# Kernel tuning notes

Hardware: AMD Instinct MI355X
Metric: run time of the kernel (lower is better)

Reference implementation:

```python
import jax, jax.numpy as jnp
import numpy as np

N_GRIDS = 64
N_FEATURES = 2
GRID_SHAPE = (64, 64, 64)  # (D, H, W)
N_DIMS = 3
N_POINTS = 262144


def setup_inputs() -> dict:
    key = jax.random.key(0)
    k1, k2, k3 = jax.random.split(key, 3)
    # Global query coordinates in [-1, 1]^3
    x = jax.random.uniform(k1, (N_POINTS, N_DIMS), dtype=jnp.float32, minval=-1.0, maxval=1.0)
    # Emulate randomize_grids(): M = (I + 0.1*U on top n_dims rows); M = M @ M^T; zero bottom-left row
    eye = jnp.eye(N_DIMS + 1, dtype=jnp.float32)[None].repeat(N_GRIDS, axis=0)
    noise = jax.random.uniform(k2, (N_GRIDS, N_DIMS, N_DIMS + 1), dtype=jnp.float32) * 0.1
    M = eye.at[:, :N_DIMS, :].add(noise)
    M = jnp.einsum('gij,gkj->gik', M, M)
    M = M.at[:, N_DIMS, :N_DIMS].set(0.0)
    # Feature grids uniform in [-1e-4, 1e-4]
    feature_grids = jax.random.uniform(
        k3, (N_GRIDS, N_FEATURES) + GRID_SHAPE, dtype=jnp.float32,
        minval=-1e-4, maxval=1e-4)
    return {"x": x, "transformation_matrices": M, "feature_grids": feature_grids}


def _trilinear_sample_one_grid(grid, coords):
    """PyTorch-style 3D grid_sample, bilinear, align_corners=True, padding_mode='zeros'.
    grid:   [F, D, H, W]
    coords: [N, 3] with last dim ordered (x, y, z) -> (W, H, D)
    returns [F, N]
    """
    F_, D, H, W = grid.shape
    # align_corners=True: map [-1,1] -> [0, size-1]
    px = (coords[:, 0] + 1.0) * 0.5 * (W - 1)
    py = (coords[:, 1] + 1.0) * 0.5 * (H - 1)
    pz = (coords[:, 2] + 1.0) * 0.5 * (D - 1)
    x0 = jnp.floor(px); y0 = jnp.floor(py); z0 = jnp.floor(pz)
    fx = px - x0; fy = py - y0; fz = pz - z0
    x0 = x0.astype(jnp.int32); y0 = y0.astype(jnp.int32); z0 = z0.astype(jnp.int32)
    out = jnp.zeros((F_, coords.shape[0]), dtype=grid.dtype)
    for dz in (0, 1):
        wz = jnp.where(dz == 1, fz, 1.0 - fz)
        iz = z0 + dz
        vz = (iz >= 0) & (iz < D)
        izc = jnp.clip(iz, 0, D - 1)
        for dy in (0, 1):
            wy = jnp.where(dy == 1, fy, 1.0 - fy)
            iy = y0 + dy
            vy = (iy >= 0) & (iy < H)
            iyc = jnp.clip(iy, 0, H - 1)
            for dx in (0, 1):
                wx = jnp.where(dx == 1, fx, 1.0 - fx)
                ix = x0 + dx
                valid = vz & vy & (ix >= 0) & (ix < W)
                ixc = jnp.clip(ix, 0, W - 1)
                vals = grid[:, izc, iyc, ixc]  # [F, N] gather
                w = (wx * wy * wz) * valid.astype(grid.dtype)
                out = out + vals * w[None, :]
    return out


def reference(x, transformation_matrices, feature_grids):
    N = x.shape[0]
    G, F_ = feature_grids.shape[0], feature_grids.shape[1]
    # transform(): homogeneous coords, batched matmul, drop homogeneous coord
    homog = jnp.concatenate([x, jnp.ones((N, 1), dtype=x.dtype)], axis=1)  # [N, 4]
    pts = jnp.einsum('gij,nj->gni', transformation_matrices, homog)[..., :N_DIMS]  # [G, N, 3]
    pts = jax.lax.stop_gradient(pts)  # forward() detaches the sampling grid
    feats = jax.vmap(_trilinear_sample_one_grid)(feature_grids, pts)  # [G, F, N]
    # flatten(0,-2).permute(1,0) -> [N, G*F]
    return feats.reshape(G * F_, N).T
```

## Files before the change

### kernel.cpp

```cpp
#include <hip/hip_runtime.h>


constexpr int NPTS  = 262144;
constexpr int GVOX  = 64 * 64 * 64;
constexpr int NCELL = 4096;

__global__ __launch_bounds__(256) void repack_kernel(
    const float* __restrict__ src, float4* __restrict__ dst)
{
    int tid = blockIdx.x * 256 + threadIdx.x;
    int g = tid >> 16;
    int q = tid & 65535;
    const float* p0 = src + (size_t)g * (2 * GVOX) + q * 4;
    float4 a = *reinterpret_cast<const float4*>(p0);
    float4 b = *reinterpret_cast<const float4*>(p0 + GVOX);
    float4* o = dst + (((size_t)g * GVOX) >> 1) + (size_t)q * 2;
    o[0] = make_float4(a.x, b.x, a.y, b.y);
    o[1] = make_float4(a.z, b.z, a.w, b.w);
}

__device__ __forceinline__ int cell_id(float x, float y, float z)
{
    int cx = min(max((int)((x + 1.0f) * 8.0f), 0), 15);
    int cy = min(max((int)((y + 1.0f) * 8.0f), 0), 15);
    int cz = min(max((int)((z + 1.0f) * 8.0f), 0), 15);
    int c = 0;
    #pragma unroll
    for (int b = 0; b < 4; ++b)
        c |= (((cx >> b) & 1) << (3 * b))
           | (((cy >> b) & 1) << (3 * b + 1))
           | (((cz >> b) & 1) << (3 * b + 2));
    return c;
}

__global__ __launch_bounds__(256) void zero_hist(int* __restrict__ hist)
{
    hist[blockIdx.x * 256 + threadIdx.x] = 0;
}

__global__ __launch_bounds__(256) void hist_kernel(
    const float* __restrict__ xs, int* __restrict__ hist)
{
    int n = blockIdx.x * 256 + threadIdx.x;
    float x = xs[n * 3 + 0], y = xs[n * 3 + 1], z = xs[n * 3 + 2];
    atomicAdd(&hist[cell_id(x, y, z)], 1);
}

__global__ __launch_bounds__(1024) void scan_kernel(
    const int* __restrict__ hist, int* __restrict__ off)
{
    __shared__ int part[1024];
    int t = threadIdx.x;
    int4 h = reinterpret_cast<const int4*>(hist)[t];
    int s = h.x + h.y + h.z + h.w;
    part[t] = s;
    __syncthreads();
    for (int d = 1; d < 1024; d <<= 1) {
        int v = (t >= d) ? part[t - d] : 0;
        __syncthreads();
        part[t] += v;
        __syncthreads();
    }
    int excl = part[t] - s;
    int4 o;
    o.x = excl;
    o.y = o.x + h.x;
    o.z = o.y + h.y;
    o.w = o.z + h.z;
    reinterpret_cast<int4*>(off)[t] = o;
}

__global__ __launch_bounds__(256) void scatter_kernel(
    const float* __restrict__ xs, int* __restrict__ off,
    float4* __restrict__ sorted)
{
    int n = blockIdx.x * 256 + threadIdx.x;
    float x = xs[n * 3 + 0], y = xs[n * 3 + 1], z = xs[n * 3 + 2];
    int c = cell_id(x, y, z);
    int pos = atomicAdd(&off[c], 1);
    sorted[pos] = make_float4(x, y, z, __int_as_float(n));
}

template <bool PACKED>
__global__ __launch_bounds__(256) void sample_sorted(
    const float4* __restrict__ sorted, const float* __restrict__ Ms,
    const float* __restrict__ grids, float* __restrict__ out)
{
    int blk = blockIdx.x;
    int chunk = ((blk & 7) << 7) + (blk >> 3);

    float4 sp = sorted[chunk * 256 + threadIdx.x];
    const float cx = sp.x, cy = sp.y, cz = sp.z;
    const int n = __float_as_int(sp.w);
    float4* outr = reinterpret_cast<float4*>(out + (size_t)n * 128);

    for (int p = 0; p < 8; ++p) {
        float2 acc[8];
        #pragma unroll
        for (int gg = 0; gg < 8; ++gg) {
            const int g = p * 8 + gg;
            const float* Mg = Ms + g * 16;
            const float px = (fmaf(Mg[0], cx, fmaf(Mg[1], cy, fmaf(Mg[2],  cz, Mg[3])))  + 1.0f) * 31.5f;
            const float py = (fmaf(Mg[4], cx, fmaf(Mg[5], cy, fmaf(Mg[6],  cz, Mg[7])))  + 1.0f) * 31.5f;
            const float pz = (fmaf(Mg[8], cx, fmaf(Mg[9], cy, fmaf(Mg[10], cz, Mg[11]))) + 1.0f) * 31.5f;

            const float flx = floorf(px), fly = floorf(py), flz = floorf(pz);
            const float fx = px - flx, fy = py - fly, fz = pz - flz;
            const int x0 = (int)flx, y0 = (int)fly, z0 = (int)flz;

            const float wx0 = (x0 >= 0  && x0 < 64) ? (1.0f - fx) : 0.0f;
            const float wx1 = (x0 >= -1 && x0 < 63) ? fx          : 0.0f;
            const float wy0 = (y0 >= 0  && y0 < 64) ? (1.0f - fy) : 0.0f;
            const float wy1 = (y0 >= -1 && y0 < 63) ? fy          : 0.0f;
            const float wz0 = (z0 >= 0  && z0 < 64) ? (1.0f - fz) : 0.0f;
            const float wz1 = (z0 >= -1 && z0 < 63) ? fz          : 0.0f;

            const int xc0 = min(max(x0, 0), 63), xc1 = min(max(x0 + 1, 0), 63);
            const int yc0 = min(max(y0, 0), 63), yc1 = min(max(y0 + 1, 0), 63);
            const int zc0 = min(max(z0, 0), 63), zc1 = min(max(z0 + 1, 0), 63);

            const int r00 = (zc0 * 64 + yc0) * 64, r01 = (zc0 * 64 + yc1) * 64;
            const int r10 = (zc1 * 64 + yc0) * 64, r11 = (zc1 * 64 + yc1) * 64;

            const float waa = wz0 * wy0, wab = wz0 * wy1;
            const float wba = wz1 * wy0, wbb = wz1 * wy1;
            const float pA0 = waa * wx0, pA1 = waa * wx1;
            const float pB0 = wab * wx0, pB1 = wab * wx1;
            const float pC0 = wba * wx0, pC1 = wba * wx1;
            const float pD0 = wbb * wx0, pD1 = wbb * wx1;

            float a0, a1;
            if constexpr (PACKED) {
                const float2* gp = reinterpret_cast<const float2*>(grids) + (size_t)g * GVOX;
                const float2 vA0 = gp[r00 + xc0], vA1 = gp[r00 + xc1];
                const float2 vB0 = gp[r01 + xc0], vB1 = gp[r01 + xc1];
                const float2 vC0 = gp[r10 + xc0], vC1 = gp[r10 + xc1];
                const float2 vD0 = gp[r11 + xc0], vD1 = gp[r11 + xc1];
                a0 = vA0.x * pA0 + vA1.x * pA1 + vB0.x * pB0 + vB1.x * pB1
                   + vC0.x * pC0 + vC1.x * pC1 + vD0.x * pD0 + vD1.x * pD1;
                a1 = vA0.y * pA0 + vA1.y * pA1 + vB0.y * pB0 + vB1.y * pB1
                   + vC0.y * pC0 + vC1.y * pC1 + vD0.y * pD0 + vD1.y * pD1;
            } else {
                const float* g0 = grids + (size_t)g * 2 * GVOX;
                const float* g1 = g0 + GVOX;
                a0 = g0[r00 + xc0] * pA0 + g0[r00 + xc1] * pA1
                   + g0[r01 + xc0] * pB0 + g0[r01 + xc1] * pB1
                   + g0[r10 + xc0] * pC0 + g0[r10 + xc1] * pC1
                   + g0[r11 + xc0] * pD0 + g0[r11 + xc1] * pD1;
                a1 = g1[r00 + xc0] * pA0 + g1[r00 + xc1] * pA1
                   + g1[r01 + xc0] * pB0 + g1[r01 + xc1] * pB1
                   + g1[r10 + xc0] * pC0 + g1[r10 + xc1] * pC1
                   + g1[r11 + xc0] * pD0 + g1[r11 + xc1] * pD1;
            }
            acc[gg] = make_float2(a0, a1);
        }
        outr[p * 4 + 0] = make_float4(acc[0].x, acc[0].y, acc[1].x, acc[1].y);
        outr[p * 4 + 1] = make_float4(acc[2].x, acc[2].y, acc[3].x, acc[3].y);
        outr[p * 4 + 2] = make_float4(acc[4].x, acc[4].y, acc[5].x, acc[5].y);
        outr[p * 4 + 3] = make_float4(acc[6].x, acc[6].y, acc[7].x, acc[7].y);
    }
}

template <bool PACKED>
__global__ __launch_bounds__(256) void sample_kernel(
    const float* __restrict__ xs, const float* __restrict__ Ms,
    const float* __restrict__ grids, float* __restrict__ out)
{
    const int g   = threadIdx.x & 63;
    const int wid = threadIdx.x >> 6;
    const float* Mg = Ms + g * 16;
    const float m00 = Mg[0], m01 = Mg[1], m02 = Mg[2],  m03 = Mg[3];
    const float m10 = Mg[4], m11 = Mg[5], m12 = Mg[6],  m13 = Mg[7];
    const float m20 = Mg[8], m21 = Mg[9], m22 = Mg[10], m23 = Mg[11];
    const float2* __restrict__ gp = reinterpret_cast<const float2*>(grids) + (size_t)g * GVOX;
    const float*  __restrict__ g0 = grids + (size_t)g * 2 * GVOX;
    const float*  __restrict__ g1 = g0 + GVOX;
    const int n0 = blockIdx.x * 32 + wid * 8;
    #pragma unroll
    for (int i = 0; i < 8; ++i) {
        const int n = n0 + i;
        const float cx = xs[n * 3 + 0], cy = xs[n * 3 + 1], cz = xs[n * 3 + 2];
        const float px = (fmaf(m00, cx, fmaf(m01, cy, fmaf(m02, cz, m03))) + 1.0f) * 31.5f;
        const float py = (fmaf(m10, cx, fmaf(m11, cy, fmaf(m12, cz, m13))) + 1.0f) * 31.5f;
        const float pz = (fmaf(m20, cx, fmaf(m21, cy, fmaf(m22, cz, m23))) + 1.0f) * 31.5f;
        const float flx = floorf(px), fly = floorf(py), flz = floorf(pz);
        const float fx = px - flx, fy = py - fly, fz = pz - flz;
        const int x0 = (int)flx, y0 = (int)fly, z0 = (int)flz;
        const float wx0 = (x0 >= 0  && x0 < 64) ? (1.0f - fx) : 0.0f;
        const float wx1 = (x0 >= -1 && x0 < 63) ? fx          : 0.0f;
        const float wy0 = (y0 >= 0  && y0 < 64) ? (1.0f - fy) : 0.0f;
        const float wy1 = (y0 >= -1 && y0 < 63) ? fy          : 0.0f;
        const float wz0 = (z0 >= 0  && z0 < 64) ? (1.0f - fz) : 0.0f;
        const float wz1 = (z0 >= -1 && z0 < 63) ? fz          : 0.0f;
        const int xc0 = min(max(x0, 0), 63), xc1 = min(max(x0 + 1, 0), 63);
        const int yc0 = min(max(y0, 0), 63), yc1 = min(max(y0 + 1, 0), 63);
        const int zc0 = min(max(z0, 0), 63), zc1 = min(max(z0 + 1, 0), 63);
        const int r00 = (zc0 * 64 + yc0) * 64, r01 = (zc0 * 64 + yc1) * 64;
        const int r10 = (zc1 * 64 + yc0) * 64, r11 = (zc1 * 64 + yc1) * 64;
        const float waa = wz0 * wy0, wab = wz0 * wy1;
        const float wba = wz1 * wy0, wbb = wz1 * wy1;
        const float pA0 = waa * wx0, pA1 = waa * wx1;
        const float pB0 = wab * wx0, pB1 = wab * wx1;
        const float pC0 = wba * wx0, pC1 = wba * wx1;
        const float pD0 = wbb * wx0, pD1 = wbb * wx1;
        float acc0, acc1;
        if constexpr (PACKED) {
            const float2 vA0 = gp[r00 + xc0], vA1 = gp[r00 + xc1];
            const float2 vB0 = gp[r01 + xc0], vB1 = gp[r01 + xc1];
            const float2 vC0 = gp[r10 + xc0], vC1 = gp[r10 + xc1];
            const float2 vD0 = gp[r11 + xc0], vD1 = gp[r11 + xc1];
            acc0 = vA0.x * pA0 + vA1.x * pA1 + vB0.x * pB0 + vB1.x * pB1
                 + vC0.x * pC0 + vC1.x * pC1 + vD0.x * pD0 + vD1.x * pD1;
            acc1 = vA0.y * pA0 + vA1.y * pA1 + vB0.y * pB0 + vB1.y * pB1
                 + vC0.y * pC0 + vC1.y * pC1 + vD0.y * pD0 + vD1.y * pD1;
        } else {
            acc0 = g0[r00 + xc0] * pA0 + g0[r00 + xc1] * pA1
                 + g0[r01 + xc0] * pB0 + g0[r01 + xc1] * pB1
                 + g0[r10 + xc0] * pC0 + g0[r10 + xc1] * pC1
                 + g0[r11 + xc0] * pD0 + g0[r11 + xc1] * pD1;
            acc1 = g1[r00 + xc0] * pA0 + g1[r00 + xc1] * pA1
                 + g1[r01 + xc0] * pB0 + g1[r01 + xc1] * pB1
                 + g1[r10 + xc0] * pC0 + g1[r10 + xc1] * pC1
                 + g1[r11 + xc0] * pD0 + g1[r11 + xc1] * pD1;
        }
        *reinterpret_cast<float2*>(out + (size_t)n * 128 + g * 2) =
            make_float2(acc0, acc1);
    }
}

extern "C" void kernel_launch(void* const* d_in, const int* in_sizes, int n_in,
                              void* d_out, int out_size, void* d_ws, size_t ws_size,
                              hipStream_t stream)
{
    const float* xs = (const float*)d_in[0];
    const float* Ms = (const float*)d_in[1];
    const float* fg = (const float*)d_in[2];
    float* out = (float*)d_out;
    char* ws = (char*)d_ws;

    const size_t SORTED_BYTES = (size_t)NPTS * 16;
    const size_t HIST_OFF = SORTED_BYTES;
    const size_t OFF_OFF  = HIST_OFF + (size_t)NCELL * 4;
    const size_t PACK_OFF = (size_t)8 << 20;
    const size_t PACK_BYTES = (size_t)64 * GVOX * 8;

    const bool can_sort = ws_size >= PACK_OFF;
    const bool can_pack_sorted = ws_size >= PACK_OFF + PACK_BYTES;
    const bool can_pack_plain  = ws_size >= PACK_BYTES;

    if (can_sort) {
        int* hist = (int*)(ws + HIST_OFF);
        int* off  = (int*)(ws + OFF_OFF);
        float4* sorted = (float4*)ws;
        zero_hist<<<16, 256, 0, stream>>>(hist);
        hist_kernel<<<NPTS / 256, 256, 0, stream>>>(xs, hist);
        scan_kernel<<<1, 1024, 0, stream>>>(hist, off);
        scatter_kernel<<<NPTS / 256, 256, 0, stream>>>(xs, off, sorted);
        if (can_pack_sorted) {
            repack_kernel<<<16384, 256, 0, stream>>>(fg, (float4*)(ws + PACK_OFF));
            sample_sorted<true><<<NPTS / 256, 256, 0, stream>>>(
                sorted, Ms, (const float*)(ws + PACK_OFF), out);
        } else {
            sample_sorted<false><<<NPTS / 256, 256, 0, stream>>>(
                sorted, Ms, fg, out);
        }
    } else if (can_pack_plain) {
        repack_kernel<<<16384, 256, 0, stream>>>(fg, (float4*)d_ws);
        sample_kernel<true><<<NPTS / 32, 256, 0, stream>>>(
            xs, Ms, (const float*)d_ws, out);
    } else {
        sample_kernel<false><<<NPTS / 32, 256, 0, stream>>>(xs, Ms, fg, out);
    }
}
```

Before: 597.6 us.

## Split grids across blockIdx.y, use paired float4 gathers and nontemporal stores

Sorted-point sampling now launches four times as many blocks. Each block handles 16 grids for its 256 points instead of one block looping over all 64, which adds parallelism and lets each block write its output in one pass. In the packed path, the two adjacent x-voxels along a row are read with a single 16-byte load per row instead of two 8-byte loads, and selects handle the border cases. Output goes through nontemporal stores, and the histogram-zeroing kernel is replaced by hipMemsetAsync. Costs are a redundant reload of each point per grid split and worse cache locality for the sorted points across y-blocks.

```diff
diff --git a/kernel.cpp b/kernel.cpp
--- a/kernel.cpp
+++ b/kernel.cpp
@@ -4,6 +4,9 @@
 constexpr int NPTS  = 262144;
 constexpr int GVOX  = 64 * 64 * 64;
 constexpr int NCELL = 4096;
+constexpr int GSPLIT = 4;
+
+typedef float f32x4 __attribute__((ext_vector_type(4)));
 
 __global__ __launch_bounds__(256) void repack_kernel(
     const float* __restrict__ src, float4* __restrict__ dst)
@@ -31,11 +34,6 @@
            | (((cy >> b) & 1) << (3 * b + 1))
            | (((cz >> b) & 1) << (3 * b + 2));
     return c;
-}
-
-__global__ __launch_bounds__(256) void zero_hist(int* __restrict__ hist)
-{
-    hist[blockIdx.x * 256 + threadIdx.x] = 0;
 }
 
 __global__ __launch_bounds__(256) void hist_kernel(
@@ -86,78 +84,98 @@
     const float4* __restrict__ sorted, const float* __restrict__ Ms,
     const float* __restrict__ grids, float* __restrict__ out)
 {
-    int blk = blockIdx.x;
-    int chunk = ((blk & 7) << 7) + (blk >> 3);
-
-    float4 sp = sorted[chunk * 256 + threadIdx.x];
+    const int blk = blockIdx.x;
+    const int chunk = ((blk & 7) << 7) + (blk >> 3);
+    const int gbase = blockIdx.y * 16;
+
+    const float4 sp = sorted[chunk * 256 + threadIdx.x];
     const float cx = sp.x, cy = sp.y, cz = sp.z;
     const int n = __float_as_int(sp.w);
-    float4* outr = reinterpret_cast<float4*>(out + (size_t)n * 128);
-
-    for (int p = 0; p < 8; ++p) {
-        float2 acc[8];
-        #pragma unroll
-        for (int gg = 0; gg < 8; ++gg) {
-            const int g = p * 8 + gg;
-            const float* Mg = Ms + g * 16;
-            const float px = (fmaf(Mg[0], cx, fmaf(Mg[1], cy, fmaf(Mg[2],  cz, Mg[3])))  + 1.0f) * 31.5f;
-            const float py = (fmaf(Mg[4], cx, fmaf(Mg[5], cy, fmaf(Mg[6],  cz, Mg[7])))  + 1.0f) * 31.5f;
-            const float pz = (fmaf(Mg[8], cx, fmaf(Mg[9], cy, fmaf(Mg[10], cz, Mg[11]))) + 1.0f) * 31.5f;
-
-            const float flx = floorf(px), fly = floorf(py), flz = floorf(pz);
-            const float fx = px - flx, fy = py - fly, fz = pz - flz;
-            const int x0 = (int)flx, y0 = (int)fly, z0 = (int)flz;
-
-            const float wx0 = (x0 >= 0  && x0 < 64) ? (1.0f - fx) : 0.0f;
-            const float wx1 = (x0 >= -1 && x0 < 63) ? fx          : 0.0f;
-            const float wy0 = (y0 >= 0  && y0 < 64) ? (1.0f - fy) : 0.0f;
-            const float wy1 = (y0 >= -1 && y0 < 63) ? fy          : 0.0f;
-            const float wz0 = (z0 >= 0  && z0 < 64) ? (1.0f - fz) : 0.0f;
-            const float wz1 = (z0 >= -1 && z0 < 63) ? fz          : 0.0f;
-
-            const int xc0 = min(max(x0, 0), 63), xc1 = min(max(x0 + 1, 0), 63);
-            const int yc0 = min(max(y0, 0), 63), yc1 = min(max(y0 + 1, 0), 63);
-            const int zc0 = min(max(z0, 0), 63), zc1 = min(max(z0 + 1, 0), 63);
-
-            const int r00 = (zc0 * 64 + yc0) * 64, r01 = (zc0 * 64 + yc1) * 64;
-            const int r10 = (zc1 * 64 + yc0) * 64, r11 = (zc1 * 64 + yc1) * 64;
-
-            const float waa = wz0 * wy0, wab = wz0 * wy1;
-            const float wba = wz1 * wy0, wbb = wz1 * wy1;
+
+    float2 acc[16];
+
+    #pragma unroll
+    for (int gg = 0; gg < 16; ++gg) {
+        const int g = gbase + gg;
+        const float* Mg = Ms + g * 16;
+        const float px = (fmaf(Mg[0], cx, fmaf(Mg[1], cy, fmaf(Mg[2],  cz, Mg[3])))  + 1.0f) * 31.5f;
+        const float py = (fmaf(Mg[4], cx, fmaf(Mg[5], cy, fmaf(Mg[6],  cz, Mg[7])))  + 1.0f) * 31.5f;
+        const float pz = (fmaf(Mg[8], cx, fmaf(Mg[9], cy, fmaf(Mg[10], cz, Mg[11]))) + 1.0f) * 31.5f;
+
+        const float flx = floorf(px), fly = floorf(py), flz = floorf(pz);
+        const float fx = px - flx, fy = py - fly, fz = pz - flz;
+        const int x0 = (int)flx, y0 = (int)fly, z0 = (int)flz;
+
+        const float wx0 = (x0 >= 0  && x0 < 64) ? (1.0f - fx) : 0.0f;
+        const float wx1 = (x0 >= -1 && x0 < 63) ? fx          : 0.0f;
+        const float wy0 = (y0 >= 0  && y0 < 64) ? (1.0f - fy) : 0.0f;
+        const float wy1 = (y0 >= -1 && y0 < 63) ? fy          : 0.0f;
+        const float wz0 = (z0 >= 0  && z0 < 64) ? (1.0f - fz) : 0.0f;
+        const float wz1 = (z0 >= -1 && z0 < 63) ? fz          : 0.0f;
+
+        const int yc0 = min(max(y0, 0), 63), yc1 = min(max(y0 + 1, 0), 63);
+        const int zc0 = min(max(z0, 0), 63), zc1 = min(max(z0 + 1, 0), 63);
+        const int r00 = (zc0 * 64 + yc0) * 64, r01 = (zc0 * 64 + yc1) * 64;
+        const int r10 = (zc1 * 64 + yc0) * 64, r11 = (zc1 * 64 + yc1) * 64;
+
+        const float waa = wz0 * wy0, wab = wz0 * wy1;
+        const float wba = wz1 * wy0, wbb = wz1 * wy1;
+
+        float a0, a1;
+        if constexpr (PACKED) {
+            const int xa = min(max(x0, 0), 62);
+            const bool hiSel = (x0 >= 63);
+            const bool loSel = (x0 < 0);
+            const float2* gp = reinterpret_cast<const float2*>(grids) + (size_t)g * GVOX;
+
+            const float4 vA = *reinterpret_cast<const float4*>(gp + (r00 + xa));
+            const float4 vB = *reinterpret_cast<const float4*>(gp + (r01 + xa));
+            const float4 vC = *reinterpret_cast<const float4*>(gp + (r10 + xa));
+            const float4 vD = *reinterpret_cast<const float4*>(gp + (r11 + xa));
+
+            const float2 cA0 = hiSel ? make_float2(vA.z, vA.w) : make_float2(vA.x, vA.y);
+            const float2 cA1 = loSel ? make_float2(vA.x, vA.y) : make_float2(vA.z, vA.w);
+            const float2 cB0 = hiSel ? make_float2(vB.z, vB.w) : make_float2(vB.x, vB.y);
+            const float2 cB1 = loSel ? make_float2(vB.x, vB.y) : make_float2(vB.z, vB.w);
+            const float2 cC0 = hiSel ? make_float2(vC.z, vC.w) : make_float2(vC.x, vC.y);
+            const float2 cC1 = loSel ? make_float2(vC.x, vC.y) : make_float2(vC.z, vC.w);
+            const float2 cD0 = hiSel ? make_float2(vD.z, vD.w) : make_float2(vD.x, vD.y);
+            const float2 cD1 = loSel ? make_float2(vD.x, vD.y) : make_float2(vD.z, vD.w);
+
             const float pA0 = waa * wx0, pA1 = waa * wx1;
             const float pB0 = wab * wx0, pB1 = wab * wx1;
             const float pC0 = wba * wx0, pC1 = wba * wx1;
             const float pD0 = wbb * wx0, pD1 = wbb * wx1;
 
-            float a0, a1;
-            if constexpr (PACKED) {
-                const float2* gp = reinterpret_cast<const float2*>(grids) + (size_t)g * GVOX;
-                const float2 vA0 = gp[r00 + xc0], vA1 = gp[r00 + xc1];
-                const float2 vB0 = gp[r01 + xc0], vB1 = gp[r01 + xc1];
-                const float2 vC0 = gp[r10 + xc0], vC1 = gp[r10 + xc1];
-                const float2 vD0 = gp[r11 + xc0], vD1 = gp[r11 + xc1];
-                a0 = vA0.x * pA0 + vA1.x * pA1 + vB0.x * pB0 + vB1.x * pB1
-                   + vC0.x * pC0 + vC1.x * pC1 + vD0.x * pD0 + vD1.x * pD1;
-                a1 = vA0.y * pA0 + vA1.y * pA1 + vB0.y * pB0 + vB1.y * pB1
-                   + vC0.y * pC0 + vC1.y * pC1 + vD0.y * pD0 + vD1.y * pD1;
-            } else {
-                const float* g0 = grids + (size_t)g * 2 * GVOX;
-                const float* g1 = g0 + GVOX;
-                a0 = g0[r00 + xc0] * pA0 + g0[r00 + xc1] * pA1
-                   + g0[r01 + xc0] * pB0 + g0[r01 + xc1] * pB1
-                   + g0[r10 + xc0] * pC0 + g0[r10 + xc1] * pC1
-                   + g0[r11 + xc0] * pD0 + g0[r11 + xc1] * pD1;
-                a1 = g1[r00 + xc0] * pA0 + g1[r00 + xc1] * pA1
-                   + g1[r01 + xc0] * pB0 + g1[r01 + xc1] * pB1
-                   + g1[r10 + xc0] * pC0 + g1[r10 + xc1] * pC1
-                   + g1[r11 + xc0] * pD0 + g1[r11 + xc1] * pD1;
-            }
-            acc[gg] = make_float2(a0, a1);
+            a0 = cA0.x * pA0 + cA1.x * pA1 + cB0.x * pB0 + cB1.x * pB1
+               + cC0.x * pC0 + cC1.x * pC1 + cD0.x * pD0 + cD1.x * pD1;
+            a1 = cA0.y * pA0 + cA1.y * pA1 + cB0.y * pB0 + cB1.y * pB1
+               + cC0.y * pC0 + cC1.y * pC1 + cD0.y * pD0 + cD1.y * pD1;
+        } else {
+            const int xc0 = min(max(x0, 0), 63), xc1 = min(max(x0 + 1, 0), 63);
+            const float pA0 = waa * wx0, pA1 = waa * wx1;
+            const float pB0 = wab * wx0, pB1 = wab * wx1;
+            const float pC0 = wba * wx0, pC1 = wba * wx1;
+            const float pD0 = wbb * wx0, pD1 = wbb * wx1;
+            const float* g0 = grids + (size_t)g * 2 * GVOX;
+            const float* g1 = g0 + GVOX;
+            a0 = g0[r00 + xc0] * pA0 + g0[r00 + xc1] * pA1
+               + g0[r01 + xc0] * pB0 + g0[r01 + xc1] * pB1
+               + g0[r10 + xc0] * pC0 + g0[r10 + xc1] * pC1
+               + g0[r11 + xc0] * pD0 + g0[r11 + xc1] * pD1;
+            a1 = g1[r00 + xc0] * pA0 + g1[r00 + xc1] * pA1
+               + g1[r01 + xc0] * pB0 + g1[r01 + xc1] * pB1
+               + g1[r10 + xc0] * pC0 + g1[r10 + xc1] * pC1
+               + g1[r11 + xc0] * pD0 + g1[r11 + xc1] * pD1;
         }
-        outr[p * 4 + 0] = make_float4(acc[0].x, acc[0].y, acc[1].x, acc[1].y);
-        outr[p * 4 + 1] = make_float4(acc[2].x, acc[2].y, acc[3].x, acc[3].y);
-        outr[p * 4 + 2] = make_float4(acc[4].x, acc[4].y, acc[5].x, acc[5].y);
-        outr[p * 4 + 3] = make_float4(acc[6].x, acc[6].y, acc[7].x, acc[7].y);
+        acc[gg] = make_float2(a0, a1);
+    }
+
+    f32x4* outr = reinterpret_cast<f32x4*>(out + (size_t)n * 128 + gbase * 2);
+    #pragma unroll
+    for (int q = 0; q < 8; ++q) {
+        f32x4 v = { acc[2 * q].x, acc[2 * q].y, acc[2 * q + 1].x, acc[2 * q + 1].y };
+        __builtin_nontemporal_store(v, &outr[q]);
     }
 }
 
@@ -252,16 +270,16 @@
         int* hist = (int*)(ws + HIST_OFF);
         int* off  = (int*)(ws + OFF_OFF);
         float4* sorted = (float4*)ws;
-        zero_hist<<<16, 256, 0, stream>>>(hist);
+        (void)hipMemsetAsync(hist, 0, NCELL * 4, stream);
         hist_kernel<<<NPTS / 256, 256, 0, stream>>>(xs, hist);
         scan_kernel<<<1, 1024, 0, stream>>>(hist, off);
         scatter_kernel<<<NPTS / 256, 256, 0, stream>>>(xs, off, sorted);
         if (can_pack_sorted) {
             repack_kernel<<<16384, 256, 0, stream>>>(fg, (float4*)(ws + PACK_OFF));
-            sample_sorted<true><<<NPTS / 256, 256, 0, stream>>>(
+            sample_sorted<true><<<dim3(NPTS / 256, GSPLIT), 256, 0, stream>>>(
                 sorted, Ms, (const float*)(ws + PACK_OFF), out);
         } else {
-            sample_sorted<false><<<NPTS / 256, 256, 0, stream>>>(
+            sample_sorted<false><<<dim3(NPTS / 256, GSPLIT), 256, 0, stream>>>(
                 sorted, Ms, fg, out);
         }
     } else if (can_pack_plain) {
```

Measured after the change: 547.5 us. 1.09x faster.
